# Kernel tuning notes

Measured on AMD Instinct MI355X. Metric: run time of the kernel, lower is better.

Reference implementation:

```python
import jax, jax.numpy as jnp
import numpy as np

H, W = 512, 512          # resized_height, resized_width
R = 2                    # cdist norm order
B, NGT = 4, 64
MAX_DIST = float(np.sqrt(H ** 2 + W ** 2))
EPS = 1e-6


def setup_inputs() -> dict:
    key = jax.random.key(0)
    k1, k2, k3, k4 = jax.random.split(key, 4)
    prob_map = jax.random.uniform(k1, (B, H, W), dtype=jnp.float32)
    # all entries > 0.2 so the torch filter prob_y[prob_y>0.2] keeps every point
    prob_y = 0.2 + 0.79 * jax.random.uniform(k2, (B, NGT), dtype=jnp.float32)
    gt = jax.random.uniform(k3, (B, NGT, 2), dtype=jnp.float32) * jnp.array([H - 1, W - 1], jnp.float32)
    orig_sizes = jax.random.randint(k4, (B, 2), 512, 2048, dtype=jnp.int32)
    return {"prob_map": prob_map, "prob_y": prob_y, "gt": gt, "orig_sizes": orig_sizes}


def _pixel_locations():
    # cartesian([arange(H), arange(W)]) -> (H*W, 2), row-major
    ii, jj = jnp.meshgrid(jnp.arange(H), jnp.arange(W), indexing="ij")
    return jnp.stack([ii, jj], axis=-1).reshape(-1, 2).astype(jnp.float32)


def _ghd(prob_map, prob_y, gt, orig_sizes):
    locs = _pixel_locations()                      # (P, 2), P = H*W
    resized = jnp.array([H, W], jnp.float32)

    def per_batch(pm, py, g, osz):
        nf = osz.astype(jnp.float32) / resized     # (2,) norm factor
        nx = nf * locs                             # (P, 2)
        ny = nf * g                                # (G, 2)
        diff = jnp.abs(nx[:, None, :] - ny[None, :, :])   # (P, G, 2)
        d = jnp.sum(diff ** R, axis=-1) ** (1.0 / R)      # (P, G)
        p = pm.reshape(-1)                         # (P,)
        n_est_pts = jnp.sum(p)
        n_gt_sum = jnp.sum(jnp.where(py > 0.2, py, 0.0))
        weighted = p[:, None] * py[None, :] * d    # p_x * p_y * d
        term_1 = jnp.sum(jnp.min(weighted, axis=1)) / (n_est_pts + EPS)
        dense = (1.0 - p[:, None]) * MAX_DIST + weighted
        term_2 = jnp.sum(jnp.min(dense, axis=0)) / (n_gt_sum + EPS)
        return term_1, term_2

    t1, t2 = jax.vmap(per_batch)(prob_map, prob_y, gt, orig_sizes)
    return t1.mean() + t2.mean()


def reference(prob_map, prob_y, gt, orig_sizes):
    return _ghd(prob_map, prob_y, gt, orig_sizes)
```

## Files before the change

### kernel.cpp

```cpp
#include <hip/hip_runtime.h>
#include <math.h>

#define HH 512
#define WW 512
#define PP (HH * WW)
#define GG 64
#define BB 4
#define THREADS 256
#define TILE 1024
#define NT (PP / TILE)
#define MAX_DIST 724.0773439350246f
#define EPSV 1e-6f


__launch_bounds__(THREADS)
__global__ void ghd_main(const float* __restrict__ prob_map,
                         const float* __restrict__ prob_y,
                         const float* __restrict__ gt,
                         const int*   __restrict__ osz,
                         float*       __restrict__ ws) {
    const int t    = blockIdx.x;
    const int b    = blockIdx.y;
    const int tid  = threadIdx.x;
    const int lane = tid & 63;
    const int wave = tid >> 6;

    __shared__ float4 gdat[GG];
    __shared__ float4 sdat[TILE];
    __shared__ float  wmin[4][GG];
    __shared__ float  s_t1[4], s_ne[4];

    const float nf0 = (float)osz[2 * b]     * (1.0f / HH);
    const float nf1 = (float)osz[2 * b + 1] * (1.0f / WW);

    if (tid < GG) {
        float py = prob_y[b * GG + tid];
        gdat[tid] = make_float4(nf0 * gt[(b * GG + tid) * 2],
                                nf1 * gt[(b * GG + tid) * 2 + 1],
                                py, py * py);
    }

    const int   pid0 = t * TILE + tid * 4;
    const float4 p4  = ((const float4*)(prob_map + (size_t)b * PP))[pid0 >> 2];
    const float nx0  = nf0 * (float)(pid0 >> 9);
    const float j0   = (float)(pid0 & (WW - 1));
    const float nx1a = nf1 * j0;
    const float nx1b = nf1 * (j0 + 1.0f);
    const float nx1c = nf1 * (j0 + 2.0f);
    const float nx1d = nf1 * (j0 + 3.0f);
    const float bsa = fmaf(-p4.x, MAX_DIST, MAX_DIST);
    const float bsb = fmaf(-p4.y, MAX_DIST, MAX_DIST);
    const float bsc = fmaf(-p4.z, MAX_DIST, MAX_DIST);
    const float bsd = fmaf(-p4.w, MAX_DIST, MAX_DIST);
    sdat[tid * 4 + 0] = make_float4(nx0, nx1a, p4.x, bsa);
    sdat[tid * 4 + 1] = make_float4(nx0, nx1b, p4.y, bsb);
    sdat[tid * 4 + 2] = make_float4(nx0, nx1c, p4.z, bsc);
    sdat[tid * 4 + 3] = make_float4(nx0, nx1d, p4.w, bsd);
    __syncthreads();

    float ma = 3.4e38f, mb = 3.4e38f, mc = 3.4e38f, md = 3.4e38f;
#pragma unroll 16
    for (int g = 0; g < GG; ++g) {
        float4 gd  = gdat[g];
        float  dx  = nx0 - gd.x;
        float  dx2 = dx * dx;
        float  da = nx1a - gd.y, db = nx1b - gd.y;
        float  dc = nx1c - gd.y, dd = nx1d - gd.y;
        ma = fminf(ma, gd.w * fmaf(da, da, dx2));
        mb = fminf(mb, gd.w * fmaf(db, db, dx2));
        mc = fminf(mc, gd.w * fmaf(dc, dc, dx2));
        md = fminf(md, gd.w * fmaf(dd, dd, dx2));
    }
    float t1 = p4.x * __builtin_amdgcn_sqrtf(ma) + p4.y * __builtin_amdgcn_sqrtf(mb)
             + p4.z * __builtin_amdgcn_sqrtf(mc) + p4.w * __builtin_amdgcn_sqrtf(md);
    float ne = p4.x + p4.y + p4.z + p4.w;

    const float4 gme = gdat[lane];
    float gmin = 3.4e38f;
    const float4* __restrict__ tp = &sdat[wave * (TILE / 4)];
#pragma unroll 4
    for (int k = 0; k < TILE / 4; k += 4) {
        float4 x0 = tp[k], x1 = tp[k + 1], x2 = tp[k + 2], x3 = tp[k + 3];
        float mbse = fminf(fminf(x0.w, x1.w), fminf(x2.w, x3.w));
        if (!__all(mbse >= gmin)) {
            float d0x = x0.x - gme.x, d0y = x0.y - gme.y;
            float d1x = x1.x - gme.x, d1y = x1.y - gme.y;
            float d2x = x2.x - gme.x, d2y = x2.y - gme.y;
            float d3x = x3.x - gme.x, d3y = x3.y - gme.y;
            float e0 = __builtin_amdgcn_sqrtf(fmaf(d0x, d0x, d0y * d0y));
            float e1 = __builtin_amdgcn_sqrtf(fmaf(d1x, d1x, d1y * d1y));
            float e2 = __builtin_amdgcn_sqrtf(fmaf(d2x, d2x, d2y * d2y));
            float e3 = __builtin_amdgcn_sqrtf(fmaf(d3x, d3x, d3y * d3y));
            gmin = fminf(gmin, fmaf(x0.z * gme.z, e0, x0.w));
            gmin = fminf(gmin, fmaf(x1.z * gme.z, e1, x1.w));
            gmin = fminf(gmin, fmaf(x2.z * gme.z, e2, x2.w));
            gmin = fminf(gmin, fmaf(x3.z * gme.z, e3, x3.w));
        }
    }
    wmin[wave][lane] = gmin;

#pragma unroll
    for (int off = 1; off < 64; off <<= 1) {
        t1 += __shfl_xor(t1, off);
        ne += __shfl_xor(ne, off);
    }
    if (lane == 0) { s_t1[wave] = t1; s_ne[wave] = ne; }
    __syncthreads();

    if (tid == 0) {
        ws[256  + b * NT + t] = s_t1[0] + s_t1[1] + s_t1[2] + s_t1[3];
        ws[1280 + b * NT + t] = s_ne[0] + s_ne[1] + s_ne[2] + s_ne[3];
    }
    if (tid < GG) {
        float v = fminf(fminf(wmin[0][tid], wmin[1][tid]),
                        fminf(wmin[2][tid], wmin[3][tid]));
        atomicMin(reinterpret_cast<unsigned*>(ws) + b * GG + tid, __float_as_uint(v));
    }
}

__global__ void ghd_final(const float* __restrict__ prob_y,
                          const float* __restrict__ ws,
                          float*       __restrict__ out) {
    const int tid = threadIdx.x;
    const int b = tid >> 6;
    const int g = tid & 63;

    float mv  = __uint_as_float(reinterpret_cast<const unsigned*>(ws)[b * GG + g]);
    float py  = prob_y[b * GG + g];
    float pyf = (py > 0.2f) ? py : 0.0f;

    float4 tv = ((const float4*)(ws + 256))[b * (NT / 4) + g];
    float4 nv = ((const float4*)(ws + 1280))[b * (NT / 4) + g];
    float t1s = tv.x + tv.y + tv.z + tv.w;
    float nes = nv.x + nv.y + nv.z + nv.w;

#pragma unroll
    for (int off = 1; off < 64; off <<= 1) {
        mv  += __shfl_xor(mv, off);
        pyf += __shfl_xor(pyf, off);
        t1s += __shfl_xor(t1s, off);
        nes += __shfl_xor(nes, off);
    }
    __shared__ float res[4];
    if (g == 0) res[b] = t1s / (nes + EPSV) + mv / (pyf + EPSV);
    __syncthreads();
    if (tid == 0) out[0] = 0.25f * (res[0] + res[1] + res[2] + res[3]);
}

extern "C" void kernel_launch(void* const* d_in, const int* in_sizes, int n_in,
                              void* d_out, int out_size, void* d_ws, size_t ws_size,
                              hipStream_t stream) {
    const float* prob_map = (const float*)d_in[0];
    const float* prob_y   = (const float*)d_in[1];
    const float* gt       = (const float*)d_in[2];
    const int*   osz      = (const int*)d_in[3];
    float* out = (float*)d_out;
    float* ws  = (float*)d_ws;

    hipMemsetAsync(ws, 0x7f, BB * GG * sizeof(unsigned), stream);

    dim3 grid(NT, BB);
    ghd_main<<<grid, THREADS, 0, stream>>>(prob_map, prob_y, gt, osz, ws);
    ghd_final<<<1, 256, 0, stream>>>(prob_y, ws, out);
}
```

Measured before the change: 93.38 us.

## Double block threads, store only probabilities in LDS, recompute coordinates in term-2 loop

Each block now uses 512 threads handling 2 pixels each instead of 256 handling 4. The shared tile shrinks from float4 records to plain probabilities, and the term-2 loop recomputes pixel coordinates and the (1-p)*MAX_DIST bias on the fly using incremental column indices. The wave-uniform early-skip branch is dropped in favour of a branch-free loop with two independent min accumulators. This trades LDS traffic and footprint for extra ALU work and loses the pruning that skipped whole chunks.

```diff
diff --git a/kernel.cpp b/kernel.cpp
--- a/kernel.cpp
+++ b/kernel.cpp
@@ -6,14 +6,15 @@
 #define PP (HH * WW)
 #define GG 64
 #define BB 4
-#define THREADS 256
+#define THREADS 512
 #define TILE 1024
 #define NT (PP / TILE)
 #define MAX_DIST 724.0773439350246f
 #define EPSV 1e-6f
+#define BIGF 3.4e38f
 
 
-__launch_bounds__(THREADS)
+__launch_bounds__(THREADS, 8)
 __global__ void ghd_main(const float* __restrict__ prob_map,
                          const float* __restrict__ prob_y,
                          const float* __restrict__ gt,
@@ -26,9 +27,9 @@
     const int wave = tid >> 6;
 
     __shared__ float4 gdat[GG];
-    __shared__ float4 sdat[TILE];
-    __shared__ float  wmin[4][GG];
-    __shared__ float  s_t1[4], s_ne[4];
+    __shared__ __align__(16) float sp[TILE];
+    __shared__ float  wmin[8][GG];
+    __shared__ float  s_t1[8], s_ne[8];
 
     const float nf0 = (float)osz[2 * b]     * (1.0f / HH);
     const float nf1 = (float)osz[2 * b + 1] * (1.0f / WW);
@@ -39,65 +40,54 @@
                                 nf1 * gt[(b * GG + tid) * 2 + 1],
                                 py, py * py);
     }
-
-    const int   pid0 = t * TILE + tid * 4;
-    const float4 p4  = ((const float4*)(prob_map + (size_t)b * PP))[pid0 >> 2];
-    const float nx0  = nf0 * (float)(pid0 >> 9);
-    const float j0   = (float)(pid0 & (WW - 1));
-    const float nx1a = nf1 * j0;
-    const float nx1b = nf1 * (j0 + 1.0f);
-    const float nx1c = nf1 * (j0 + 2.0f);
-    const float nx1d = nf1 * (j0 + 3.0f);
-    const float bsa = fmaf(-p4.x, MAX_DIST, MAX_DIST);
-    const float bsb = fmaf(-p4.y, MAX_DIST, MAX_DIST);
-    const float bsc = fmaf(-p4.z, MAX_DIST, MAX_DIST);
-    const float bsd = fmaf(-p4.w, MAX_DIST, MAX_DIST);
-    sdat[tid * 4 + 0] = make_float4(nx0, nx1a, p4.x, bsa);
-    sdat[tid * 4 + 1] = make_float4(nx0, nx1b, p4.y, bsb);
-    sdat[tid * 4 + 2] = make_float4(nx0, nx1c, p4.z, bsc);
-    sdat[tid * 4 + 3] = make_float4(nx0, nx1d, p4.w, bsd);
+    ((float2*)sp)[tid] = ((const float2*)(prob_map + (size_t)b * PP + t * TILE))[tid];
     __syncthreads();
 
-    float ma = 3.4e38f, mb = 3.4e38f, mc = 3.4e38f, md = 3.4e38f;
+    const int   pid0 = t * TILE + tid * 2;
+    const float p0 = sp[tid * 2], p1 = sp[tid * 2 + 1];
+    const float nx0  = nf0 * (float)(pid0 >> 9);
+    const float nx1a = nf1 * (float)(pid0 & (WW - 1));
+    float ma = BIGF, mb = BIGF;
 #pragma unroll 16
     for (int g = 0; g < GG; ++g) {
         float4 gd  = gdat[g];
         float  dx  = nx0 - gd.x;
         float  dx2 = dx * dx;
-        float  da = nx1a - gd.y, db = nx1b - gd.y;
-        float  dc = nx1c - gd.y, dd = nx1d - gd.y;
+        float  da  = nx1a - gd.y;
+        float  db  = da + nf1;
         ma = fminf(ma, gd.w * fmaf(da, da, dx2));
         mb = fminf(mb, gd.w * fmaf(db, db, dx2));
-        mc = fminf(mc, gd.w * fmaf(dc, dc, dx2));
-        md = fminf(md, gd.w * fmaf(dd, dd, dx2));
     }
-    float t1 = p4.x * __builtin_amdgcn_sqrtf(ma) + p4.y * __builtin_amdgcn_sqrtf(mb)
-             + p4.z * __builtin_amdgcn_sqrtf(mc) + p4.w * __builtin_amdgcn_sqrtf(md);
-    float ne = p4.x + p4.y + p4.z + p4.w;
+    float t1 = p0 * __builtin_amdgcn_sqrtf(ma) + p1 * __builtin_amdgcn_sqrtf(mb);
+    float ne = p0 + p1;
 
-    const float4 gme = gdat[lane];
-    float gmin = 3.4e38f;
-    const float4* __restrict__ tp = &sdat[wave * (TILE / 4)];
-#pragma unroll 4
-    for (int k = 0; k < TILE / 4; k += 4) {
-        float4 x0 = tp[k], x1 = tp[k + 1], x2 = tp[k + 2], x3 = tp[k + 3];
-        float mbse = fminf(fminf(x0.w, x1.w), fminf(x2.w, x3.w));
-        if (!__all(mbse >= gmin)) {
-            float d0x = x0.x - gme.x, d0y = x0.y - gme.y;
-            float d1x = x1.x - gme.x, d1y = x1.y - gme.y;
-            float d2x = x2.x - gme.x, d2y = x2.y - gme.y;
-            float d3x = x3.x - gme.x, d3y = x3.y - gme.y;
-            float e0 = __builtin_amdgcn_sqrtf(fmaf(d0x, d0x, d0y * d0y));
-            float e1 = __builtin_amdgcn_sqrtf(fmaf(d1x, d1x, d1y * d1y));
-            float e2 = __builtin_amdgcn_sqrtf(fmaf(d2x, d2x, d2y * d2y));
-            float e3 = __builtin_amdgcn_sqrtf(fmaf(d3x, d3x, d3y * d3y));
-            gmin = fminf(gmin, fmaf(x0.z * gme.z, e0, x0.w));
-            gmin = fminf(gmin, fmaf(x1.z * gme.z, e1, x1.w));
-            gmin = fminf(gmin, fmaf(x2.z * gme.z, e2, x2.w));
-            gmin = fminf(gmin, fmaf(x3.z * gme.z, e3, x3.w));
-        }
+    const float4 gme  = gdat[lane];
+    const int    s0   = wave * (TILE / 8);
+    const int    pidw = t * TILE + s0;
+    const float  dxw  = nf0 * (float)(pidw >> 9) - gme.x;
+    const float  dx2w = dxw * dxw;
+    const float  mgy  = -gme.y;
+    float jf  = (float)(pidw & (WW - 1));
+    float gm0 = BIGF, gm1 = BIGF;
+    const float4* __restrict__ sp4 = (const float4*)(sp + s0);
+#pragma unroll 8
+    for (int k = 0; k < TILE / 8 / 4; ++k) {
+        float4 q = sp4[k];
+        float dy0 = fmaf(nf1, jf,        mgy);
+        float dy1 = fmaf(nf1, jf + 1.0f, mgy);
+        float dy2 = fmaf(nf1, jf + 2.0f, mgy);
+        float dy3 = fmaf(nf1, jf + 3.0f, mgy);
+        float e0 = __builtin_amdgcn_sqrtf(fmaf(dy0, dy0, dx2w));
+        float e1 = __builtin_amdgcn_sqrtf(fmaf(dy1, dy1, dx2w));
+        float e2 = __builtin_amdgcn_sqrtf(fmaf(dy2, dy2, dx2w));
+        float e3 = __builtin_amdgcn_sqrtf(fmaf(dy3, dy3, dx2w));
+        gm0 = fminf(gm0, fmaf(q.x * gme.z, e0, fmaf(-q.x, MAX_DIST, MAX_DIST)));
+        gm1 = fminf(gm1, fmaf(q.y * gme.z, e1, fmaf(-q.y, MAX_DIST, MAX_DIST)));
+        gm0 = fminf(gm0, fmaf(q.z * gme.z, e2, fmaf(-q.z, MAX_DIST, MAX_DIST)));
+        gm1 = fminf(gm1, fmaf(q.w * gme.z, e3, fmaf(-q.w, MAX_DIST, MAX_DIST)));
+        jf += 4.0f;
     }
-    wmin[wave][lane] = gmin;
+    wmin[wave][lane] = fminf(gm0, gm1);
 
 #pragma unroll
     for (int off = 1; off < 64; off <<= 1) {
@@ -108,12 +98,16 @@
     __syncthreads();
 
     if (tid == 0) {
-        ws[256  + b * NT + t] = s_t1[0] + s_t1[1] + s_t1[2] + s_t1[3];
-        ws[1280 + b * NT + t] = s_ne[0] + s_ne[1] + s_ne[2] + s_ne[3];
+        float st = 0.0f, sn = 0.0f;
+#pragma unroll
+        for (int w = 0; w < 8; ++w) { st += s_t1[w]; sn += s_ne[w]; }
+        ws[256  + b * NT + t] = st;
+        ws[1280 + b * NT + t] = sn;
     }
     if (tid < GG) {
-        float v = fminf(fminf(wmin[0][tid], wmin[1][tid]),
-                        fminf(wmin[2][tid], wmin[3][tid]));
+        float v = wmin[0][tid];
+#pragma unroll
+        for (int w = 1; w < 8; ++w) v = fminf(v, wmin[w][tid]);
         atomicMin(reinterpret_cast<unsigned*>(ws) + b * GG + tid, __float_as_uint(v));
     }
 }
```

New measurement: 86.44 us. 7.4% less time.
